# Optimization experiments

Measured on AMD Instinct MI355X. Metric: run time of the kernel, lower is better.

## Reference

```python
import math
import jax, jax.numpy as jnp
import numpy as np

EPS = 1e-12
PHYSICAL_EPS = 1e-18
MAX_MOMENT = 0.05
PARTICLE_MOMENT = 1e-14
DRAG = 1e-16
STATIC_FRICTION = 1e-19
MIN_DWELL = 0.01
MAX_DWELL = 0.2
RECENCY_SCALE = 0.1
RELAX_KEEP = math.exp(-RECENCY_SCALE)
N_POINTS = 65536
N_WAYPOINTS = 128
PLANE_HALF = 0.01  # meters
Z_MIN, Z_MAX = 0.002, 0.01


def setup_inputs() -> dict:
    key = jax.random.key(0)
    k1, k2, k3, k4, k5 = jax.random.split(key, 5)
    # evaluation points on the z=0 imaging plane
    pts_xy = (jax.random.uniform(k1, (N_POINTS, 2)) - 0.5) * (2.0 * PLANE_HALF)
    points = jnp.concatenate([pts_xy, jnp.zeros((N_POINTS, 1))], axis=-1)
    # waypoint dipole centers above the plane
    c_xy = (jax.random.uniform(k2, (N_WAYPOINTS, 2)) - 0.5) * (2.0 * PLANE_HALF)
    c_z = Z_MIN + (Z_MAX - Z_MIN) * jax.random.uniform(k3, (N_WAYPOINTS, 1))
    centers = jnp.concatenate([c_xy, c_z], axis=-1)
    raw_moment = 0.5 * jax.random.normal(k4, (N_WAYPOINTS, 3))
    raw_dwell = 0.5 * jax.random.normal(k5, (N_WAYPOINTS,))
    return {"points": points, "centers": centers,
            "raw_moment": raw_moment, "raw_dwell": raw_dwell}


def reference(points, centers, raw_moment, raw_dwell):
    # parameter transforms (as in moment_vec / dwell_time_s)
    moments = MAX_MOMENT * jnp.tanh(raw_moment)              # [W,3]
    dwell = MIN_DWELL + (MAX_DWELL - MIN_DWELL) * jax.nn.sigmoid(raw_dwell)  # [W]

    friction_thr = STATIC_FRICTION / max(PARTICLE_MOMENT, PHYSICAL_EPS)
    moment_norm = math.sqrt(3.0) * MAX_MOMENT
    eff_r2 = (2.0 * moment_norm / friction_thr) ** (2.0 / 3.0)  # effective radius squared

    pts_xy = points[:, :2]
    pts_xy2 = jnp.sum(pts_xy * pts_xy, axis=-1)               # [N]
    N = points.shape[0]

    def step(carry, inp):
        orient, active_time, peak_bxy = carry
        c, m, dt = inp  # [3], [3], scalar
        # dipole field of this waypoint at all points
        rel = points - c                                       # [N,3]
        r2 = jnp.maximum(jnp.sum(rel * rel, axis=-1), EPS)     # [N]
        r = jnp.sqrt(r2)
        inv_r3 = 1.0 / (r2 * r)
        inv_r5 = inv_r3 / r2
        mdotr = rel @ m                                        # [N]
        field = 3.0 * rel * (mdotr * inv_r5)[:, None] - m * inv_r3[:, None]
        bmag = jnp.linalg.norm(field, axis=-1)                 # [N]
        bdir = field / jnp.maximum(bmag, EPS)[:, None]
        # candidate mask (horizontal effective-radius test)
        hr2 = jnp.maximum(eff_r2 - c[2] * c[2], 0.0)
        dxy2 = pts_xy2 + jnp.sum(c[:2] * c[:2]) - 2.0 * (pts_xy @ c[:2])
        cand = dxy2 <= hr2                                     # [N] bool
        # exact_align_vectors
        cross = jnp.cross(orient, bdir)                        # [N,3]
        sin_t = jnp.clip(jnp.linalg.norm(cross, axis=-1), 0.0, 1.0)
        cos_t = jnp.clip(jnp.sum(orient * bdir, axis=-1), -1.0, 1.0)
        torque = PARTICLE_MOMENT * bmag * sin_t
        active = torque > STATIC_FRICTION
        rate = PARTICLE_MOMENT * bmag / max(DRAG, PHYSICAL_EPS)
        tan_half = sin_t / jnp.maximum(1.0 + cos_t, EPS)
        theta = jnp.arctan2(sin_t, cos_t)
        theta_new = 2.0 * jnp.arctan(tan_half * jnp.exp(-rate * dt))
        rot = jnp.where(active, jnp.clip(theta - theta_new, 0.0, math.pi), 0.0)
        # rotate_vectors(orient, cross, rot)
        axis_norm = jnp.linalg.norm(cross, axis=-1, keepdims=True)
        unit = cross / jnp.maximum(axis_norm, EPS)
        ca = jnp.cos(rot)[:, None]
        sa = jnp.sin(rot)[:, None]
        rotated = (orient * ca
                   + jnp.cross(unit, orient) * sa
                   + unit * jnp.sum(unit * orient, axis=-1, keepdims=True) * (1.0 - ca))
        new_orient = jnp.where(axis_norm > 1e-6, rotated, orient)
        new_orient = jnp.where(cand[:, None], new_orient, orient)
        # per-point accumulators
        active_time = active_time + jnp.where(cand & active, dt, 0.0)
        bxy = jnp.linalg.norm(field[:, :2], axis=-1)
        peak_bxy = jnp.maximum(peak_bxy * RELAX_KEEP, jnp.where(cand, bxy, 0.0))
        return (new_orient, active_time, peak_bxy), None

    orient0 = jnp.broadcast_to(jnp.array([0.0, 0.0, 1.0], dtype=points.dtype), (N, 3))
    zeros = jnp.zeros((N,), dtype=points.dtype)
    (orient, active_time, peak_bxy), _ = jax.lax.scan(
        step, (orient0, zeros, zeros), (centers, moments, dwell))
    return jnp.concatenate(
        [orient, active_time[:, None], peak_bxy[:, None]], axis=-1)  # [N,5]
```

## Files before the change

### kernel.cpp

```cpp
#include <hip/hip_runtime.h>
#include <cmath>

#define NWP 128
#define BLOCK 256

__global__ void magnet_prep_r14(const float* __restrict__ centers,
                                const float* __restrict__ raw_moment,
                                const float* __restrict__ raw_dwell,
                                float4* __restrict__ wp)
{
    const int k = threadIdx.x;
    if (k < NWP) {
        const float cx = centers[3 * k + 0];
        const float cy = centers[3 * k + 1];
        const float cz = centers[3 * k + 2];
        const float mx = 0.05f * tanhf(raw_moment[3 * k + 0]);
        const float my = 0.05f * tanhf(raw_moment[3 * k + 1]);
        const float mz = 0.05f * tanhf(raw_moment[3 * k + 2]);
        const float sig = 1.0f / (1.0f + expf(-raw_dwell[k]));
        const float dtv = 0.01f + 0.19f * sig;
        const float dk = exp2f(-0.28853900817779268f * (float)(NWP - 1 - k));
        wp[2 * k + 0] = make_float4(cx, cy, cz, dtv);
        wp[2 * k + 1] = make_float4(mx, my, mz, dk);
    }
}

__global__ __launch_bounds__(BLOCK) void magnet_scan_r14(
    const float* __restrict__ points,
    const float4* __restrict__ wp,
    float* __restrict__ out,
    int n_points)
{
    const int i = blockIdx.x * BLOCK + threadIdx.x;
    if (i >= n_points) return;

    const float px = points[3 * i + 0];
    const float py = points[3 * i + 1];

    float gpx = 0.0f, gpy = 0.0f, gpz = 1.0f, b2p = 1.0f;
    float gsx = 0.0f, gsy = 0.0f, gsz = 1.0f, b2s = 1.0f;
    float at = 0.0f, peak2 = 0.0f;

    #pragma unroll 8
    for (int k = 0; k < NWP; ++k) {
        const float4 w0 = wp[2 * k + 0];
        const float4 w1 = wp[2 * k + 1];
        const float cx = w0.x, cy = w0.y, cz = w0.z, dtv = w0.w;
        const float mx = w1.x, my = w1.y, mz = w1.z, dk = w1.w;

        const float rx = px - cx, ry = py - cy;
        const float r2 = fmaf(rx, rx, fmaf(ry, ry, cz * cz));
        const float mdotr = fmaf(mz, -cz, fmaf(my, ry, mx * rx));
        const float t3 = 3.0f * mdotr;
        const float gx = fmaf(t3, rx, -(mx * r2));
        const float gy = fmaf(t3, ry, -(my * r2));
        const float gz = fmaf(t3, -cz, -(mz * r2));
        const float bxy2g = fmaf(gy, gy, gx * gx);
        const float b2g = fmaf(gz, gz, bxy2g);

        const float pr = __builtin_amdgcn_rcpf(r2);
        const float p2 = pr * pr;
        const float S = p2 * p2 * pr;

        peak2 = fmaxf(peak2, (bxy2g * S) * dk);

        const float ux = fmaf(gpy, gz, -(gpz * gy));
        const float uy = fmaf(gpz, gx, -(gpx * gz));
        const float uz = fmaf(gpx, gy, -(gpy * gx));
        const float X2 = fmaf(uz, uz, fmaf(uy, uy, ux * ux));

        const bool active = X2 * S > 1e-10f * b2p;
        const bool use_rot = active && (X2 > 1e-12f * (b2g * b2p));

        gsx = use_rot ? gx : gsx;
        gsy = use_rot ? gy : gsy;
        gsz = use_rot ? gz : gsz;
        b2s = use_rot ? b2g : b2s;
        at += active ? dtv : 0.0f;

        gpx = gx; gpy = gy; gpz = gz; b2p = b2g;
    }

    const float inv = __builtin_amdgcn_rsqf(b2s);
    out[5 * i + 0] = gsx * inv;
    out[5 * i + 1] = gsy * inv;
    out[5 * i + 2] = gsz * inv;
    out[5 * i + 3] = at;
    out[5 * i + 4] = sqrtf(peak2);
}

extern "C" void kernel_launch(void* const* d_in, const int* in_sizes, int n_in,
                              void* d_out, int out_size, void* d_ws, size_t ws_size,
                              hipStream_t stream) {
    const float* points = (const float*)d_in[0];
    const float* centers = (const float*)d_in[1];
    const float* raw_moment = (const float*)d_in[2];
    const float* raw_dwell = (const float*)d_in[3];
    float* out = (float*)d_out;
    float4* wp = (float4*)d_ws;

    const int n_points = in_sizes[0] / 3;

    magnet_prep_r14<<<1, NWP, 0, stream>>>(centers, raw_moment, raw_dwell, wp);

    const int grid = (n_points + BLOCK - 1) / BLOCK;
    magnet_scan_r14<<<grid, BLOCK, 0, stream>>>(points, wp, out, n_points);
}
```

Measured before the change: 76.09 us.

## Split waypoint scan into four segments per point and fuse prep kernel

Each point's 128-step scan is split across four threads, each covering 32 waypoints. Each segment seeds its previous-field state by recomputing the field of the waypoint just before it, and the partial results (last fired orientation, summed active time, max peak) are merged through shared memory. The parameter-transform prep kernel is folded into the scan kernel, with per-block waypoint tables held in LDS, which removes one launch. The grid becomes four times larger with shorter serial chains. In exchange, every block recomputes the tanh/sigmoid transforms and adds two barriers plus a combine step.

```diff
diff --git a/kernel.cpp b/kernel.cpp
--- a/kernel.cpp
+++ b/kernel.cpp
@@ -2,49 +2,73 @@
 #include <cmath>
 
 #define NWP 128
+#define NSEG 4
+#define SEGLEN 32
+#define PTS 64
 #define BLOCK 256
 
-__global__ void magnet_prep_r14(const float* __restrict__ centers,
-                                const float* __restrict__ raw_moment,
-                                const float* __restrict__ raw_dwell,
-                                float4* __restrict__ wp)
-{
-    const int k = threadIdx.x;
-    if (k < NWP) {
-        const float cx = centers[3 * k + 0];
-        const float cy = centers[3 * k + 1];
-        const float cz = centers[3 * k + 2];
-        const float mx = 0.05f * tanhf(raw_moment[3 * k + 0]);
-        const float my = 0.05f * tanhf(raw_moment[3 * k + 1]);
-        const float mz = 0.05f * tanhf(raw_moment[3 * k + 2]);
-        const float sig = 1.0f / (1.0f + expf(-raw_dwell[k]));
-        const float dtv = 0.01f + 0.19f * sig;
-        const float dk = exp2f(-0.28853900817779268f * (float)(NWP - 1 - k));
-        wp[2 * k + 0] = make_float4(cx, cy, cz, dtv);
-        wp[2 * k + 1] = make_float4(mx, my, mz, dk);
-    }
-}
-
-__global__ __launch_bounds__(BLOCK) void magnet_scan_r14(
+__global__ __launch_bounds__(BLOCK, 4) void magnet_scan_r16(
     const float* __restrict__ points,
-    const float4* __restrict__ wp,
+    const float* __restrict__ centers,
+    const float* __restrict__ raw_moment,
+    const float* __restrict__ raw_dwell,
     float* __restrict__ out,
     int n_points)
 {
-    const int i = blockIdx.x * BLOCK + threadIdx.x;
-    if (i >= n_points) return;
+    __shared__ float4 s_w0[NWP];
+    __shared__ float4 s_w1[NWP];
+    __shared__ float4 sh_a[NSEG][PTS];
+    __shared__ float2 sh_b[NSEG][PTS];
 
-    const float px = points[3 * i + 0];
-    const float py = points[3 * i + 1];
+    const int t = threadIdx.x;
+    if (t < NWP) {
+        const float cx = centers[3 * t + 0];
+        const float cy = centers[3 * t + 1];
+        const float cz = centers[3 * t + 2];
+        const float mx = 0.05f * tanhf(raw_moment[3 * t + 0]);
+        const float my = 0.05f * tanhf(raw_moment[3 * t + 1]);
+        const float mz = 0.05f * tanhf(raw_moment[3 * t + 2]);
+        const float sig = 1.0f / (1.0f + expf(-raw_dwell[t]));
+        const float dtv = 0.01f + 0.19f * sig;
+        const float dk = exp2f(-0.28853900817779268f * (float)(NWP - 1 - t));
+        s_w0[t] = make_float4(cx, cy, cz, dtv);
+        s_w1[t] = make_float4(mx, my, mz, dk);
+    }
+    __syncthreads();
+
+    const int pt = t & (PTS - 1);
+    const int seg = t >> 6;
+    int p = blockIdx.x * PTS + pt;
+    const bool valid = p < n_points;
+    p = valid ? p : (n_points - 1);
+
+    const float px = points[3 * p + 0];
+    const float py = points[3 * p + 1];
+
+    const int kbase = seg * SEGLEN;
 
     float gpx = 0.0f, gpy = 0.0f, gpz = 1.0f, b2p = 1.0f;
+    if (seg != 0) {
+        const float4 w0 = s_w0[kbase - 1];
+        const float4 w1 = s_w1[kbase - 1];
+        const float rx = px - w0.x, ry = py - w0.y;
+        const float r2 = fmaf(rx, rx, fmaf(ry, ry, w0.z * w0.z));
+        const float mdotr = fmaf(w1.z, -w0.z, fmaf(w1.y, ry, w1.x * rx));
+        const float t3 = 3.0f * mdotr;
+        gpx = fmaf(t3, rx, -(w1.x * r2));
+        gpy = fmaf(t3, ry, -(w1.y * r2));
+        gpz = fmaf(t3, -w0.z, -(w1.z * r2));
+        b2p = fmaf(gpz, gpz, fmaf(gpy, gpy, gpx * gpx));
+    }
+
     float gsx = 0.0f, gsy = 0.0f, gsz = 1.0f, b2s = 1.0f;
-    float at = 0.0f, peak2 = 0.0f;
+    float at = 0.0f, peak2 = 0.0f, fired = 0.0f;
 
     #pragma unroll 8
-    for (int k = 0; k < NWP; ++k) {
-        const float4 w0 = wp[2 * k + 0];
-        const float4 w1 = wp[2 * k + 1];
+    for (int kk = 0; kk < SEGLEN; ++kk) {
+        const int k = kbase + kk;
+        const float4 w0 = s_w0[k];
+        const float4 w1 = s_w1[k];
         const float cx = w0.x, cy = w0.y, cz = w0.z, dtv = w0.w;
         const float mx = w1.x, my = w1.y, mz = w1.z, dk = w1.w;
 
@@ -76,17 +100,39 @@
         gsy = use_rot ? gy : gsy;
         gsz = use_rot ? gz : gsz;
         b2s = use_rot ? b2g : b2s;
+        fired = use_rot ? 1.0f : fired;
         at += active ? dtv : 0.0f;
 
         gpx = gx; gpy = gy; gpz = gz; b2p = b2g;
     }
 
     const float inv = __builtin_amdgcn_rsqf(b2s);
-    out[5 * i + 0] = gsx * inv;
-    out[5 * i + 1] = gsy * inv;
-    out[5 * i + 2] = gsz * inv;
-    out[5 * i + 3] = at;
-    out[5 * i + 4] = sqrtf(peak2);
+    sh_a[seg][pt] = make_float4(gsx * inv, gsy * inv, gsz * inv, at);
+    sh_b[seg][pt] = make_float2(peak2, fired);
+    __syncthreads();
+
+    if (t < PTS) {
+        float pk2 = 0.0f, atot = 0.0f;
+        float fox = 0.0f, foy = 0.0f, foz = 1.0f;
+        #pragma unroll
+        for (int s = 0; s < NSEG; ++s) {
+            const float4 a4 = sh_a[s][t];
+            const float2 b2v = sh_b[s][t];
+            pk2 = fmaxf(pk2, b2v.x);
+            atot += a4.w;
+            const bool f = b2v.y != 0.0f;
+            fox = f ? a4.x : fox;
+            foy = f ? a4.y : foy;
+            foz = f ? a4.z : foz;
+        }
+        if (valid) {
+            out[5 * p + 0] = fox;
+            out[5 * p + 1] = foy;
+            out[5 * p + 2] = foz;
+            out[5 * p + 3] = atot;
+            out[5 * p + 4] = sqrtf(pk2);
+        }
+    }
 }
 
 extern "C" void kernel_launch(void* const* d_in, const int* in_sizes, int n_in,
@@ -97,12 +143,11 @@
     const float* raw_moment = (const float*)d_in[2];
     const float* raw_dwell = (const float*)d_in[3];
     float* out = (float*)d_out;
-    float4* wp = (float4*)d_ws;
+    (void)d_ws; (void)ws_size;
 
     const int n_points = in_sizes[0] / 3;
 
-    magnet_prep_r14<<<1, NWP, 0, stream>>>(centers, raw_moment, raw_dwell, wp);
-
-    const int grid = (n_points + BLOCK - 1) / BLOCK;
-    magnet_scan_r14<<<grid, BLOCK, 0, stream>>>(points, wp, out, n_points);
+    const int grid = (n_points + PTS - 1) / PTS;
+    magnet_scan_r16<<<grid, BLOCK, 0, stream>>>(points, centers, raw_moment,
+                                                raw_dwell, out, n_points);
 }
```

Measured after the change: 69.88 us. 1.09x faster.
